# Performance work log

Hardware: AMD Instinct MI355X
Metric: run time of the kernel (lower is better)

Reference implementation:

```python
import jax, jax.numpy as jnp
import numpy as np

RBF_CO = 10.077141124806595


def setup_inputs() -> dict:
    key = jax.random.key(0)
    k1, k2, k3 = jax.random.split(key, 3)
    n, dim = 2048, 128
    N, out_dim = 50000, 64
    features = jax.random.normal(k1, (n, dim), dtype=jnp.float32)
    train_data = jax.random.normal(k2, (N, dim), dtype=jnp.float32)
    weights = jax.random.normal(k3, (N, out_dim), dtype=jnp.float32) * 0.02
    return {"features": features, "train_data": train_data, "weights": weights}


def reference(features, train_data, weights):
    x2 = jnp.sum(features * features, axis=-1, keepdims=True)      # [n, 1]
    t2 = jnp.sum(train_data * train_data, axis=-1)                 # [N]
    d2 = x2 + t2[None, :] - 2.0 * (features @ train_data.T)        # [n, N]
    dist = jnp.sqrt(jnp.maximum(d2, 0.0))                          # clamp fp error
    k = jnp.exp(-dist / RBF_CO / 2.0)                              # RBF kernel [n, N]
    return k @ weights                                              # [n, out_dim]
```

## Files before the change

kernel.cpp:

```cpp
#include <hip/hip_runtime.h>
#include <hip/hip_bf16.h>
#include <stdint.h>

#define DIM 128
#define ODIM 64
#define BM 128
#define BN 64
#define NSPLIT 48

typedef __attribute__((ext_vector_type(8))) __bf16 bf16x8;
typedef __attribute__((ext_vector_type(2))) __bf16 bf16x2;
typedef __attribute__((ext_vector_type(4))) float f32x4;
typedef __attribute__((ext_vector_type(2))) unsigned int uint32x2;
typedef __attribute__((ext_vector_type(4))) unsigned int uint32x4;

#define MFMA16(a, b, c) __builtin_amdgcn_mfma_f32_16x16x32_bf16((a), (b), (c), 0, 0, 0)

#define RBFD 10.077141124806595
#define LOG2E 1.4426950408889634
#define C2D ((LOG2E / (2.0 * RBFD)) * (LOG2E / (2.0 * RBFD)))

__device__ __forceinline__ void async_copy16(const void* g, void* l) {
  __builtin_amdgcn_global_load_lds((const __attribute__((address_space(1))) void*)g,
                                   (__attribute__((address_space(3))) void*)l, 16, 0, 0);
}

__device__ __forceinline__ uint32_t pack_bf16(float a, float b) {
  uint32_t ua = __builtin_bit_cast(uint32_t, a) + 0x8000u;
  uint32_t ub = __builtin_bit_cast(uint32_t, b) + 0x8000u;
  return __builtin_amdgcn_perm(ub, ua, 0x07060302u);
}

__global__ void prep_all(const float* __restrict__ train, __bf16* __restrict__ Tb,
                         float* __restrict__ t2, const float* __restrict__ feat,
                         __bf16* __restrict__ Fb, float* __restrict__ x2,
                         const float* __restrict__ W, __bf16* __restrict__ Wt,
                         int Ntrain, int Npad, int nFeat,
                         int trainBlocks, int rowBlocks, float scale) {
  __shared__ float tile[64][65];
  const int b = (int)blockIdx.x;
  const int t = (int)threadIdx.x;

  if (b < rowBlocks) {
    const float* src;
    __bf16* dst;
    float* sq;
    int nValid, nPad, row0;
    float padv;
    if (b < trainBlocks) {
      src = train; dst = Tb; sq = t2; nValid = Ntrain; nPad = Npad; row0 = b * 4; padv = 1e30f;
    } else {
      src = feat; dst = Fb; sq = x2; nValid = nFeat; nPad = nFeat; row0 = (b - trainBlocks) * 4; padv = 0.0f;
    }
    int row = row0 + (t >> 6);
    int lane = t & 63;
    if (row >= nPad) return;
    float2 v = make_float2(0.0f, 0.0f);
    if (row < nValid) v = ((const float2*)src)[(size_t)row * 64 + lane];
    bf16x2 p;
    p.x = (__bf16)v.x;
    p.y = (__bf16)v.y;
    *(bf16x2*)&dst[(size_t)row * DIM + lane * 2] = p;
    float ss = v.x * v.x + v.y * v.y;
    #pragma unroll
    for (int off = 32; off > 0; off >>= 1) ss += __shfl_down(ss, off);
    if (lane == 0) sq[row] = (row < nValid) ? ss * scale : padv;
    return;
  }

  int j0 = (b - rowBlocks) * 64;
  int jr = t >> 2;
  int cg = (t & 3) * 16;
  int j = j0 + jr;
  if (j < Ntrain) {
    const float4* src = (const float4*)(W + (size_t)j * ODIM);
    #pragma unroll
    for (int q = 0; q < 4; ++q) {
      float4 u = src[(cg >> 2) + q];
      tile[jr][cg + q * 4 + 0] = u.x;
      tile[jr][cg + q * 4 + 1] = u.y;
      tile[jr][cg + q * 4 + 2] = u.z;
      tile[jr][cg + q * 4 + 3] = u.w;
    }
  } else {
    #pragma unroll
    for (int q = 0; q < 16; ++q) tile[jr][cg + q] = 0.0f;
  }
  __syncthreads();
  int v = t >> 2;
  int jc = (t & 3) * 16;
  __bf16 ob[16];
  #pragma unroll
  for (int q = 0; q < 16; ++q) ob[q] = (__bf16)tile[jc + q][v];
  __bf16* dst = Wt + (size_t)v * Npad + j0 + jc;
  *(bf16x8*)dst = *(bf16x8*)&ob[0];
  *(bf16x8*)(dst + 8) = *(bf16x8*)&ob[8];
}

template <bool ATOMIC>
__global__ __launch_bounds__(256, 3) void rbf_main(
    const __bf16* __restrict__ Fb, const __bf16* __restrict__ Tb,
    const __bf16* __restrict__ Wt, const float* __restrict__ t2g,
    const float* __restrict__ x2g, float* __restrict__ outOrPart,
    int nRows, int Npad, int nChunks) {
  __shared__ __bf16 sT[2][BN * DIM];
  __shared__ __bf16 sW[2][ODIM * BN];

  const int tid = threadIdx.x;
  const int wave = tid >> 6;
  const int lane = tid & 63;
  const int l16 = lane & 15;
  const int g4 = lane >> 4;

  const int ns = (int)blockIdx.x;
  const int mb = (int)blockIdx.y;

  constexpr float KNEG2 = (float)(-2.0 * C2D);

  bf16x8 bF[2][4];
  #pragma unroll
  for (int nf = 0; nf < 2; ++nf)
    #pragma unroll
    for (int ko = 0; ko < 4; ++ko)
      bF[nf][ko] = *(const bf16x8*)(Fb + ((size_t)(mb * BM + wave * 32 + nf * 16 + l16)) * DIM +
                                    ko * 32 + g4 * 8);

  float x2v[2];
  #pragma unroll
  for (int nf = 0; nf < 2; ++nf)
    x2v[nf] = x2g[mb * BM + wave * 32 + nf * 16 + l16];

  f32x4 zero4 = {0.0f, 0.0f, 0.0f, 0.0f};
  f32x4 oacc[2][4];
  #pragma unroll
  for (int mo = 0; mo < 2; ++mo)
    #pragma unroll
    for (int vi = 0; vi < 4; ++vi) oacc[mo][vi] = zero4;

  auto stage = [&](int bsel, int c) {
    const char* gT = (const char*)Tb + (size_t)c * (BN * DIM * 2);
    char* lT = (char*)&sT[bsel][0];
    #pragma unroll
    for (int i = 0; i < 4; ++i) {
      int off = i * 4096 + wave * 1024;
      int loff = off + lane * 16;
      int row = loff >> 8;
      int gran = (loff >> 4) & 15;
      async_copy16(gT + row * 256 + ((gran ^ (row & 15)) << 4), lT + off);
    }
    char* lW = (char*)&sW[bsel][0];
    #pragma unroll
    for (int i = 0; i < 2; ++i) {
      int off = i * 4096 + wave * 1024;
      int loff = off + lane * 16;
      int v = loff >> 7;
      int gran = (loff >> 4) & 7;
      const char* gW = (const char*)Wt + ((size_t)v * Npad + c * BN) * 2 + ((gran ^ (v & 7)) << 4);
      async_copy16(gW, lW + off);
    }
  };

  stage(0, ns);
  int buf = 0;

  for (int c = ns; c < nChunks; c += NSPLIT) {
    const int n0 = c * BN;
    __syncthreads();

    f32x4 t2v[4];
    #pragma unroll
    for (int mt = 0; mt < 4; ++mt)
      t2v[mt] = *(const f32x4*)(t2g + n0 + mt * 16 + g4 * 4);

    int cn = c + NSPLIT;
    if (cn < nChunks) stage(buf ^ 1, cn);

    f32x4 sacc[4][2];
    #pragma unroll
    for (int mt = 0; mt < 4; ++mt)
      #pragma unroll
      for (int nf = 0; nf < 2; ++nf) sacc[mt][nf] = zero4;

    #pragma unroll
    for (int ko = 0; ko < 4; ++ko) {
      bf16x8 a[4];
      #pragma unroll
      for (int mt = 0; mt < 4; ++mt) {
        int row = mt * 16 + l16;
        int slot = (ko * 4 + g4) ^ l16;
        a[mt] = *(const bf16x8*)((const char*)&sT[buf][0] + row * 256 + (slot << 4));
      }
      #pragma unroll
      for (int mt = 0; mt < 4; ++mt)
        #pragma unroll
        for (int nf = 0; nf < 2; ++nf)
          sacc[mt][nf] = MFMA16(a[mt], bF[nf][ko], sacc[mt][nf]);
    }

    uint32_t plo[4][2], phi[4][2];
    #pragma unroll
    for (int mt = 0; mt < 4; ++mt) {
      #pragma unroll
      for (int nf = 0; nf < 2; ++nf) {
        f32x4 s = sacc[mt][nf];
        float kv[4];
        #pragma unroll
        for (int r = 0; r < 4; ++r) {
          float d2 = __builtin_fmaf(KNEG2, s[r], t2v[mt][r] + x2v[nf]);
          d2 = fmaxf(d2, 0.0f);
          kv[r] = __builtin_amdgcn_exp2f(-__builtin_amdgcn_sqrtf(d2));
        }
        plo[mt][nf] = pack_bf16(kv[0], kv[1]);
        phi[mt][nf] = pack_bf16(kv[2], kv[3]);
      }
    }

    #pragma unroll
    for (int ko2 = 0; ko2 < 2; ++ko2) {
      bf16x8 w[4];
      #pragma unroll
      for (int vi = 0; vi < 4; ++vi) {
        int v = vi * 16 + l16;
        int slot = (ko2 * 4 + g4) ^ (l16 & 7);
        w[vi] = *(const bf16x8*)((const char*)&sW[buf][0] + v * 128 + (slot << 4));
      }
      #pragma unroll
      for (int nf = 0; nf < 2; ++nf) {
        uint32x2 rA = __builtin_amdgcn_permlane32_swap(plo[2 * ko2][nf], plo[2 * ko2 + 1][nf],
                                                       false, false);
        uint32x2 rB = __builtin_amdgcn_permlane16_swap(rA[0], rA[1], false, false);
        uint32x2 rC = __builtin_amdgcn_permlane32_swap(phi[2 * ko2][nf], phi[2 * ko2 + 1][nf],
                                                       false, false);
        uint32x2 rD = __builtin_amdgcn_permlane16_swap(rC[0], rC[1], false, false);
        uint32x4 pd = {rB[0], rD[0], rB[1], rD[1]};
        bf16x8 p = __builtin_bit_cast(bf16x8, pd);
        #pragma unroll
        for (int vi = 0; vi < 4; ++vi)
          oacc[nf][vi] = MFMA16(p, w[vi], oacc[nf][vi]);
      }
    }

    buf ^= 1;
  }

  if (ATOMIC) {
    float* out = outOrPart;
    #pragma unroll
    for (int mo = 0; mo < 2; ++mo)
      #pragma unroll
      for (int vi = 0; vi < 4; ++vi)
        #pragma unroll
        for (int r = 0; r < 4; ++r) {
          int row = mb * BM + wave * 32 + mo * 16 + g4 * 4 + r;
          int col = vi * 16 + l16;
          atomicAdd(&out[(size_t)row * ODIM + col], oacc[mo][vi][r]);
        }
  } else {
    float* dst = outOrPart + (size_t)ns * (size_t)nRows * ODIM;
    #pragma unroll
    for (int mo = 0; mo < 2; ++mo)
      #pragma unroll
      for (int vi = 0; vi < 4; ++vi)
        #pragma unroll
        for (int r = 0; r < 4; ++r) {
          int row = mb * BM + wave * 32 + mo * 16 + g4 * 4 + r;
          int col = vi * 16 + l16;
          dst[(size_t)row * ODIM + col] = oacc[mo][vi][r];
        }
  }
}

__global__ void reduce_parts(const float4* __restrict__ part, float4* __restrict__ out,
                             int total4) {
  int i = (int)blockIdx.x * blockDim.x + threadIdx.x;
  if (i >= total4) return;
  float4 s = make_float4(0.0f, 0.0f, 0.0f, 0.0f);
  #pragma unroll
  for (int sp = 0; sp < NSPLIT; ++sp) {
    float4 v = part[(size_t)sp * total4 + i];
    s.x += v.x; s.y += v.y; s.z += v.z; s.w += v.w;
  }
  out[i] = s;
}

extern "C" void kernel_launch(void* const* d_in, const int* in_sizes, int n_in,
                              void* d_out, int out_size, void* d_ws, size_t ws_size,
                              hipStream_t stream) {
  (void)n_in;
  const float* features = (const float*)d_in[0];
  const float* train = (const float*)d_in[1];
  const float* weights = (const float*)d_in[2];
  float* out = (float*)d_out;

  const int n = in_sizes[0] / DIM;
  const int N = in_sizes[1] / DIM;
  const int Npad = ((N + 63) / 64) * 64;
  const int nChunks = Npad / 64;

  size_t off = 0;
  auto alloc = [&](size_t bytes) {
    size_t o = off;
    off = (off + bytes + 255) & ~(size_t)255;
    return o;
  };
  size_t oT = alloc((size_t)Npad * DIM * 2);
  size_t oW = alloc((size_t)ODIM * Npad * 2);
  size_t oF = alloc((size_t)n * DIM * 2);
  size_t ot2 = alloc((size_t)Npad * 4);
  size_t ox2 = alloc((size_t)n * 4);
  size_t oPart = alloc((size_t)NSPLIT * n * ODIM * 4);
  size_t needFull = off;

  char* ws = (char*)d_ws;
  __bf16* Tb = (__bf16*)(ws + oT);
  __bf16* Wt = (__bf16*)(ws + oW);
  __bf16* Fb = (__bf16*)(ws + oF);
  float* t2 = (float*)(ws + ot2);
  float* x2 = (float*)(ws + ox2);

  const float scale = (float)C2D;
  const int trainBlocks = Npad / 4;
  const int rowBlocks = trainBlocks + n / 4;
  const int wBlocks = Npad / 64;
  prep_all<<<rowBlocks + wBlocks, 256, 0, stream>>>(train, Tb, t2, features, Fb, x2,
                                                    weights, Wt, N, Npad, n,
                                                    trainBlocks, rowBlocks, scale);

  const int mBlocks = n / BM;
  dim3 grid(NSPLIT, mBlocks);

  if (ws_size >= needFull) {
    float* part = (float*)(ws + oPart);
    rbf_main<false><<<grid, 256, 0, stream>>>(Fb, Tb, Wt, t2, x2, part, n, Npad, nChunks);
    int total4 = n * ODIM / 4;
    reduce_parts<<<(total4 + 127) / 128, 128, 0, stream>>>((const float4*)part, (float4*)out,
                                                           total4);
  } else {
    hipMemsetAsync(d_out, 0, (size_t)out_size * sizeof(float), stream);
    rbf_main<true><<<grid, 256, 0, stream>>>(Fb, Tb, Wt, t2, x2, out, n, Npad, nChunks);
  }
}
```

Baseline: 150.8 us.

## Load weight fragments directly from global, drop LDS weight staging, raise split count

The transposed weight tile is no longer staged through LDS with async copies; each lane reads its bf16x8 weight fragments straight from global memory before the second MFMA stage. This halves nothing in T staging but frees LDS so occupancy can rise to 4 blocks per CU (launch bounds raised), and the N-split count goes from 48 to 64 when workspace allows, with the reduction kernel taking a runtime split count. Direct global loads per wave are uncoalesced-ish and not prefetched, so they may add latency, and more splits increase partial-sum traffic in the reduction.

```diff
diff --git a/kernel.cpp b/kernel.cpp
--- a/kernel.cpp
+++ b/kernel.cpp
@@ -6,7 +6,6 @@
 #define ODIM 64
 #define BM 128
 #define BN 64
-#define NSPLIT 48
 
 typedef __attribute__((ext_vector_type(8))) __bf16 bf16x8;
 typedef __attribute__((ext_vector_type(2))) __bf16 bf16x2;
@@ -98,13 +97,12 @@
 }
 
 template <bool ATOMIC>
-__global__ __launch_bounds__(256, 3) void rbf_main(
+__global__ __launch_bounds__(256, 4) void rbf_main(
     const __bf16* __restrict__ Fb, const __bf16* __restrict__ Tb,
     const __bf16* __restrict__ Wt, const float* __restrict__ t2g,
     const float* __restrict__ x2g, float* __restrict__ outOrPart,
-    int nRows, int Npad, int nChunks) {
+    int nRows, int Npad, int nChunks, int nsplit) {
   __shared__ __bf16 sT[2][BN * DIM];
-  __shared__ __bf16 sW[2][ODIM * BN];
 
   const int tid = threadIdx.x;
   const int wave = tid >> 6;
@@ -148,22 +146,12 @@
       int gran = (loff >> 4) & 15;
       async_copy16(gT + row * 256 + ((gran ^ (row & 15)) << 4), lT + off);
     }
-    char* lW = (char*)&sW[bsel][0];
-    #pragma unroll
-    for (int i = 0; i < 2; ++i) {
-      int off = i * 4096 + wave * 1024;
-      int loff = off + lane * 16;
-      int v = loff >> 7;
-      int gran = (loff >> 4) & 7;
-      const char* gW = (const char*)Wt + ((size_t)v * Npad + c * BN) * 2 + ((gran ^ (v & 7)) << 4);
-      async_copy16(gW, lW + off);
-    }
   };
 
   stage(0, ns);
   int buf = 0;
 
-  for (int c = ns; c < nChunks; c += NSPLIT) {
+  for (int c = ns; c < nChunks; c += nsplit) {
     const int n0 = c * BN;
     __syncthreads();
 
@@ -172,7 +160,7 @@
     for (int mt = 0; mt < 4; ++mt)
       t2v[mt] = *(const f32x4*)(t2g + n0 + mt * 16 + g4 * 4);
 
-    int cn = c + NSPLIT;
+    int cn = c + nsplit;
     if (cn < nChunks) stage(buf ^ 1, cn);
 
     f32x4 sacc[4][2];
@@ -215,15 +203,15 @@
       }
     }
 
+    bf16x8 w[2][4];
+    #pragma unroll
+    for (int ko2 = 0; ko2 < 2; ++ko2)
+      #pragma unroll
+      for (int vi = 0; vi < 4; ++vi)
+        w[ko2][vi] = *(const bf16x8*)(Wt + (size_t)(vi * 16 + l16) * Npad + n0 + ko2 * 32 + g4 * 8);
+
     #pragma unroll
     for (int ko2 = 0; ko2 < 2; ++ko2) {
-      bf16x8 w[4];
-      #pragma unroll
-      for (int vi = 0; vi < 4; ++vi) {
-        int v = vi * 16 + l16;
-        int slot = (ko2 * 4 + g4) ^ (l16 & 7);
-        w[vi] = *(const bf16x8*)((const char*)&sW[buf][0] + v * 128 + (slot << 4));
-      }
       #pragma unroll
       for (int nf = 0; nf < 2; ++nf) {
         uint32x2 rA = __builtin_amdgcn_permlane32_swap(plo[2 * ko2][nf], plo[2 * ko2 + 1][nf],
@@ -236,7 +224,7 @@
         bf16x8 p = __builtin_bit_cast(bf16x8, pd);
         #pragma unroll
         for (int vi = 0; vi < 4; ++vi)
-          oacc[nf][vi] = MFMA16(p, w[vi], oacc[nf][vi]);
+          oacc[nf][vi] = MFMA16(p, w[ko2][vi], oacc[nf][vi]);
       }
     }
 
@@ -271,12 +259,11 @@
 }
 
 __global__ void reduce_parts(const float4* __restrict__ part, float4* __restrict__ out,
-                             int total4) {
+                             int total4, int nsplit) {
   int i = (int)blockIdx.x * blockDim.x + threadIdx.x;
   if (i >= total4) return;
   float4 s = make_float4(0.0f, 0.0f, 0.0f, 0.0f);
-  #pragma unroll
-  for (int sp = 0; sp < NSPLIT; ++sp) {
+  for (int sp = 0; sp < nsplit; ++sp) {
     float4 v = part[(size_t)sp * total4 + i];
     s.x += v.x; s.y += v.y; s.z += v.z; s.w += v.w;
   }
@@ -308,8 +295,17 @@
   size_t oF = alloc((size_t)n * DIM * 2);
   size_t ot2 = alloc((size_t)Npad * 4);
   size_t ox2 = alloc((size_t)n * 4);
-  size_t oPart = alloc((size_t)NSPLIT * n * ODIM * 4);
-  size_t needFull = off;
+  size_t oPart = alloc(0);
+  size_t fixed = off;
+
+  int nsplit = 64;
+  size_t partBytes = (size_t)nsplit * n * ODIM * 4;
+  bool haveWs = ws_size >= fixed + partBytes;
+  if (!haveWs) {
+    nsplit = 48;
+    partBytes = (size_t)nsplit * n * ODIM * 4;
+    haveWs = ws_size >= fixed + partBytes;
+  }
 
   char* ws = (char*)d_ws;
   __bf16* Tb = (__bf16*)(ws + oT);
@@ -327,16 +323,16 @@
                                                     trainBlocks, rowBlocks, scale);
 
   const int mBlocks = n / BM;
-  dim3 grid(NSPLIT, mBlocks);
-
-  if (ws_size >= needFull) {
+  dim3 grid((unsigned)(haveWs ? nsplit : 64), (unsigned)mBlocks);
+
+  if (haveWs) {
     float* part = (float*)(ws + oPart);
-    rbf_main<false><<<grid, 256, 0, stream>>>(Fb, Tb, Wt, t2, x2, part, n, Npad, nChunks);
+    rbf_main<false><<<grid, 256, 0, stream>>>(Fb, Tb, Wt, t2, x2, part, n, Npad, nChunks, nsplit);
     int total4 = n * ODIM / 4;
-    reduce_parts<<<(total4 + 127) / 128, 128, 0, stream>>>((const float4*)part, (float4*)out,
-                                                           total4);
+    reduce_parts<<<(total4 + 255) / 256, 256, 0, stream>>>((const float4*)part, (float4*)out,
+                                                           total4, nsplit);
   } else {
     hipMemsetAsync(d_out, 0, (size_t)out_size * sizeof(float), stream);
-    rbf_main<true><<<grid, 256, 0, stream>>>(Fb, Tb, Wt, t2, x2, out, n, Npad, nChunks);
-  }
-}
+    rbf_main<true><<<grid, 256, 0, stream>>>(Fb, Tb, Wt, t2, x2, out, n, Npad, nChunks, 64);
+  }
+}
```

New measurement: 189.1 us. +25.4%, slower.
